# Performance work log

Hardware: AMD Instinct MI355X
Metric: run time of the kernel (lower is better)

The kernel has to match this reference:

```python
import jax, jax.numpy as jnp
import numpy as np

B, S, H, NH = 4, 2048, 2048, 16
HD = H // NH  # 128


def setup_inputs() -> dict:
    key = jax.random.key(0)
    ks = jax.random.split(key, 9)
    s = lambda fan_in: 1.0 / np.sqrt(fan_in)
    return {
        "hidden_state": jax.random.normal(ks[0], (B, S, H), dtype=jnp.float32),
        # Linear weights stored as [in, out]
        "w_q": jax.random.uniform(ks[1], (H, H), jnp.float32, -s(H), s(H)),
        "b_q": jax.random.uniform(ks[2], (H,), jnp.float32, -s(H), s(H)),
        "w_k": jax.random.uniform(ks[3], (H, HD), jnp.float32, -s(H), s(H)),
        "b_k": jax.random.uniform(ks[4], (HD,), jnp.float32, -s(H), s(H)),
        "w_v": jax.random.uniform(ks[5], (H, HD), jnp.float32, -s(H), s(H)),
        "b_v": jax.random.uniform(ks[6], (HD,), jnp.float32, -s(H), s(H)),
        "w_o": jax.random.uniform(ks[7], (H, H), jnp.float32, -s(H), s(H)),
        "b_o": jax.random.uniform(ks[8], (H,), jnp.float32, -s(H), s(H)),
    }


def reference(hidden_state, w_q, b_q, w_k, b_k, w_v, b_v, w_o, b_o):
    b = hidden_state.shape[0]
    q = hidden_state @ w_q + b_q                       # [B,S,H]
    k = hidden_state @ w_k + b_k                       # [B,S,HD] (single KV head)
    v = hidden_state @ w_v + b_v                       # [B,S,HD]
    q = q.reshape(b, -1, NH, HD).transpose(0, 2, 1, 3)  # [B,NH,S,HD]
    scale = jnp.sqrt(jnp.float32(HD))
    scores = jnp.einsum("bhqd,bkd->bhqk", q, k) / scale  # [B,NH,S,S]
    probs = jax.nn.softmax(scores, axis=-1)
    out = jnp.einsum("bhqk,bkd->bhqd", probs, v)        # [B,NH,S,HD]
    # Faithful to original: transpose(-1,-2) (NOT transpose(1,2)) then view
    out = jnp.swapaxes(out, -1, -2).reshape(b, -1, HD * NH)  # [B,S,H]
    return out @ w_o + b_o
```

## Files before the change

### kernel.cpp

```cpp
#include <hip/hip_runtime.h>
#include <math.h>


#define BATCH 4
#define SLEN 2048
#define HDIM 2048
#define NHEADS 16
#define HD 128

typedef __bf16 bf16x8 __attribute__((ext_vector_type(8)));
typedef float f32x4 __attribute__((ext_vector_type(4)));

__device__ __forceinline__ void gload_lds16(const void* g, void* l) {
    __builtin_amdgcn_global_load_lds(
        (const __attribute__((address_space(1))) void*)g,
        (__attribute__((address_space(3))) void*)l, 16, 0, 0);
}

__device__ __forceinline__ int xcd_swizzle(int bid, int nwg) {
    int cpx = nwg >> 3;
    return (bid & 7) * cpx + (bid >> 3);
}

__global__ void conv_bf16(const float* __restrict__ in, __bf16* __restrict__ out) {
    int i = (blockIdx.x * 256 + threadIdx.x) * 8;
    float4 a = *reinterpret_cast<const float4*>(in + i);
    float4 b = *reinterpret_cast<const float4*>(in + i + 4);
    bf16x8 o;
    o[0] = (__bf16)a.x; o[1] = (__bf16)a.y; o[2] = (__bf16)a.z; o[3] = (__bf16)a.w;
    o[4] = (__bf16)b.x; o[5] = (__bf16)b.y; o[6] = (__bf16)b.z; o[7] = (__bf16)b.w;
    *reinterpret_cast<bf16x8*>(out + i) = o;
}

__global__ void transpose_conv(const float* __restrict__ in, __bf16* __restrict__ out,
                               int R, int C) {
    __shared__ float tile[32][33];
    int c0 = blockIdx.x * 32, r0 = blockIdx.y * 32;
    int tr = threadIdx.x >> 5, tc = threadIdx.x & 31;
#pragma unroll
    for (int i = 0; i < 4; ++i)
        tile[tr + i * 8][tc] = in[(size_t)(r0 + tr + i * 8) * C + c0 + tc];
    __syncthreads();
#pragma unroll
    for (int i = 0; i < 4; ++i)
        out[(size_t)(c0 + tr + i * 8) * R + r0 + tc] = (__bf16)tile[tc][tr + i * 8];
}

template <int MODE>
__global__ __launch_bounds__(256) void gemm_bt(
    const __bf16* __restrict__ A, const __bf16* __restrict__ BT,
    const float* __restrict__ bias, const float* __restrict__ bias2,
    void* __restrict__ Cout, void* __restrict__ Cout2,
    int M, int N, int K, int nbx)
{
    __shared__ __bf16 As[128 * 64];
    __shared__ __bf16 Bs[128 * 64];
    const int t = threadIdx.x;
    const int lane = t & 63;
    const int w = t >> 6;
    const int wr = w >> 1, wc = w & 1;
    const int id = xcd_swizzle(blockIdx.x, gridDim.x);
    const int m0 = (id / nbx) << 7, n0 = (id % nbx) << 7;

    f32x4 acc[4][4] = {};
    const int l8 = (lane & 7) * 8;
    const int lr = lane >> 3;

    for (int k0 = 0; k0 < K; k0 += 64) {
        __syncthreads();
#pragma unroll
        for (int i = 0; i < 4; ++i) {
            int c = w * 4 + i;
            int row = c * 8 + lr;
            gload_lds16(A + (size_t)(m0 + row) * K + k0 + l8, (char*)As + c * 1024);
            gload_lds16(BT + (size_t)(n0 + row) * K + k0 + l8, (char*)Bs + c * 1024);
        }
        __syncthreads();
#pragma unroll
        for (int ks = 0; ks < 2; ++ks) {
            bf16x8 a[4], b[4];
#pragma unroll
            for (int i = 0; i < 4; ++i) {
                a[i] = *reinterpret_cast<const bf16x8*>(
                    As + (wr * 64 + i * 16 + (lane & 15)) * 64 + ks * 32 + (lane >> 4) * 8);
                b[i] = *reinterpret_cast<const bf16x8*>(
                    Bs + (wc * 64 + i * 16 + (lane & 15)) * 64 + ks * 32 + (lane >> 4) * 8);
            }
#pragma unroll
            for (int i = 0; i < 4; ++i)
#pragma unroll
                for (int j = 0; j < 4; ++j)
                    acc[i][j] = __builtin_amdgcn_mfma_f32_16x16x32_bf16(
                        a[i], b[j], acc[i][j], 0, 0, 0);
        }
    }

    const int col_l = lane & 15, rgrp = lane >> 4;
#pragma unroll
    for (int j = 0; j < 4; ++j) {
        int col = n0 + wc * 64 + j * 16 + col_l;
        float bv;
        if (MODE == 3)
            bv = (col < HD) ? bias[col] : bias2[col - HD];
        else
            bv = bias[col];
#pragma unroll
        for (int i = 0; i < 4; ++i) {
            int rowb = m0 + wr * 64 + i * 16 + rgrp * 4;
#pragma unroll
            for (int r = 0; r < 4; ++r) {
                float v = acc[i][j][r] + bv;
                int row = rowb + r;
                if (MODE == 0)
                    ((float*)Cout)[(size_t)row * N + col] = v;
                else if (MODE == 1)
                    ((__bf16*)Cout)[(size_t)row * N + col] = (__bf16)v;
                else {
                    if (col < HD)
                        ((__bf16*)Cout)[(size_t)row * HD + col] = (__bf16)v;
                    else
                        ((__bf16*)Cout2)[((size_t)(row >> 11) * HD + (col - HD)) * SLEN
                                         + (row & (SLEN - 1))] = (__bf16)v;
                }
            }
        }
    }
}

__attribute__((amdgpu_waves_per_eu(2, 4)))
__global__ __launch_bounds__(512) void mqa_attn_mfma(
    const __bf16* __restrict__ Q,
    const __bf16* __restrict__ K,
    const __bf16* __restrict__ VT,
    __bf16* __restrict__ T)
{
    __shared__ __align__(16) __bf16 smem[40960];
    __bf16* KsB = smem;
    __bf16* VtB = smem + 16384;
    __bf16* PsB = smem + 32768;

    const int t = threadIdx.x;
    const int lane = t & 63;
    const int w = t >> 6;
    const int bid = xcd_swizzle(blockIdx.x, gridDim.x);
    const int qb = bid & 15;
    const int nh = (bid >> 4) & 15;
    const int b = bid >> 8;
    const int q0 = qb << 7;

    const int cl = lane & 15;
    const int rg = lane >> 4;

    const float scale = 0.08838834764831845f;

    bf16x8 qf[4];
    {
        const __bf16* qrow = Q + (size_t)(b * SLEN + q0 + w * 16 + cl) * HDIM
                             + nh * HD + rg * 8;
#pragma unroll
        for (int ks = 0; ks < 4; ++ks) {
            bf16x8 raw = *reinterpret_cast<const bf16x8*>(qrow + ks * 32);
#pragma unroll
            for (int j = 0; j < 8; ++j)
                qf[ks][j] = (__bf16)((float)raw[j] * scale);
        }
    }

    f32x4 O[8] = {};
    float m[4], l[4];
#pragma unroll
    for (int r = 0; r < 4; ++r) { m[r] = -__builtin_inff(); l[r] = 0.f; }

    const int k_row0 = (w * 2) * 4 + (lane >> 4);
    const int k_cc0  = lane & 15;
    const int v_row0 = (w * 2) * 8 + (lane >> 3);
    const int v_cc0  = lane & 7;

#define STAGE_KV(TILE, BUF)                                                     \
    do {                                                                        \
        int kk_ = (TILE) * 64;                                                  \
        _Pragma("unroll")                                                       \
        for (int j = 0; j < 2; ++j) {                                           \
            int idx = w * 2 + j;                                                \
            int row = k_row0 + j * 4;                                           \
            int cc  = k_cc0 ^ (row & 7);                                        \
            gload_lds16(K + (size_t)(b * SLEN + kk_ + row) * HD + cc * 8,       \
                        (char*)(KsB + (BUF) * 8192) + idx * 1024);              \
        }                                                                       \
        _Pragma("unroll")                                                       \
        for (int j = 0; j < 2; ++j) {                                           \
            int idx = w * 2 + j;                                                \
            int row = v_row0 + j * 8;                                           \
            int cc  = v_cc0 ^ (row & 7);                                        \
            gload_lds16(VT + (size_t)(b * HD + row) * SLEN + kk_ + cc * 8,      \
                        (char*)(VtB + (BUF) * 8192) + idx * 1024);              \
        }                                                                       \
    } while (0)

    STAGE_KV(0, 0);
    __syncthreads();

    int buf = 0;
    const int NT = SLEN / 64;
    for (int tt = 0; tt < NT; ++tt) {
        if (tt + 1 < NT) STAGE_KV(tt + 1, buf ^ 1);

        const __bf16* Kb_ = KsB + buf * 8192;
        const __bf16* Vb_ = VtB + buf * 8192;

        f32x4 s[4] = {};
        __builtin_amdgcn_s_setprio(1);
#pragma unroll
        for (int cb = 0; cb < 4; ++cb) {
            const int row = cb * 16 + cl;
            const __bf16* kr = Kb_ + row * 128;
            const int sw = row & 7;
#pragma unroll
            for (int ks = 0; ks < 4; ++ks) {
                bf16x8 kf = *reinterpret_cast<const bf16x8*>(
                    kr + (((ks * 4 + rg) ^ sw) << 3));
                s[cb] = __builtin_amdgcn_mfma_f32_16x16x32_bf16(qf[ks], kf, s[cb], 0, 0, 0);
            }
        }
        __builtin_amdgcn_s_setprio(0);

        float tmax[4], mx = 0.f;
#pragma unroll
        for (int r = 0; r < 4; ++r) {
            float tm = fmaxf(fmaxf(s[0][r], s[1][r]), fmaxf(s[2][r], s[3][r]));
            tm = fmaxf(tm, __shfl_xor(tm, 1));
            tm = fmaxf(tm, __shfl_xor(tm, 2));
            tm = fmaxf(tm, __shfl_xor(tm, 4));
            tm = fmaxf(tm, __shfl_xor(tm, 8));
            tmax[r] = tm;
            mx = fmaxf(mx, tm - m[r]);
        }
        if (__any(mx > 8.f)) {
#pragma unroll
            for (int r = 0; r < 4; ++r) {
                float mn = fmaxf(m[r], tmax[r]);
                float alpha = __expf(m[r] - mn);
                m[r] = mn;
                l[r] *= alpha;
#pragma unroll
                for (int dcb = 0; dcb < 8; ++dcb) O[dcb][r] *= alpha;
            }
        }
        float rs[4] = {0.f, 0.f, 0.f, 0.f};
#pragma unroll
        for (int cb = 0; cb < 4; ++cb)
#pragma unroll
            for (int r = 0; r < 4; ++r) {
                float p = __expf(s[cb][r] - m[r]);
                rs[r] += p;
                int row = rg * 4 + r;
                int col = (cb * 16 + cl) ^ ((row & 7) << 3);
                PsB[w * 1024 + row * 64 + col] = (__bf16)p;
            }
#pragma unroll
        for (int r = 0; r < 4; ++r) {
            float v = rs[r];
            v += __shfl_xor(v, 1);
            v += __shfl_xor(v, 2);
            v += __shfl_xor(v, 4);
            v += __shfl_xor(v, 8);
            l[r] += v;
        }

        bf16x8 pf[2];
#pragma unroll
        for (int ks = 0; ks < 2; ++ks)
            pf[ks] = *reinterpret_cast<const bf16x8*>(
                PsB + w * 1024 + cl * 64 + (((ks * 4 + rg) ^ (cl & 7)) << 3));
        __builtin_amdgcn_s_setprio(1);
#pragma unroll
        for (int dcb = 0; dcb < 8; ++dcb) {
            const int row = dcb * 16 + cl;
            const __bf16* vr = Vb_ + row * 64;
            const int sw = row & 7;
#pragma unroll
            for (int ks = 0; ks < 2; ++ks) {
                bf16x8 vf = *reinterpret_cast<const bf16x8*>(
                    vr + (((ks * 4 + rg) ^ sw) << 3));
                O[dcb] = __builtin_amdgcn_mfma_f32_16x16x32_bf16(pf[ks], vf, O[dcb], 0, 0, 0);
            }
        }
        __builtin_amdgcn_s_setprio(0);

        __syncthreads();
        buf ^= 1;
    }
#undef STAGE_KV

    __bf16 (*Eb)[136] = reinterpret_cast<__bf16(*)[136]>(smem);
    float invl[4];
#pragma unroll
    for (int r = 0; r < 4; ++r) invl[r] = 1.0f / l[r];
#pragma unroll
    for (int dcb = 0; dcb < 8; ++dcb)
#pragma unroll
        for (int r = 0; r < 4; ++r)
            Eb[dcb * 16 + cl][w * 16 + rg * 4 + r] = (__bf16)(O[dcb][r] * invl[r]);
    __syncthreads();
#pragma unroll
    for (int i = 0; i < 4; ++i) {
        int id = i * 512 + t;
        int d = id >> 4, c = id & 15;
        float4 v = *reinterpret_cast<const float4*>(&Eb[d][c * 8]);
        *reinterpret_cast<float4*>(
            T + (size_t)(b * HDIM + nh * HD + d) * SLEN + q0 + c * 8) = v;
    }
}

extern "C" void kernel_launch(void* const* d_in, const int* in_sizes, int n_in,
                              void* d_out, int out_size, void* d_ws, size_t ws_size,
                              hipStream_t stream) {
    const float* hs  = (const float*)d_in[0];
    const float* w_q = (const float*)d_in[1];
    const float* b_q = (const float*)d_in[2];
    const float* w_k = (const float*)d_in[3];
    const float* b_k = (const float*)d_in[4];
    const float* w_v = (const float*)d_in[5];
    const float* b_v = (const float*)d_in[6];
    const float* w_o = (const float*)d_in[7];
    const float* b_o = (const float*)d_in[8];

    const int M = BATCH * SLEN;
    const size_t MH = (size_t)M * HDIM;

    __bf16* hs_b = (__bf16*)d_out;
    __bf16* Qb   = hs_b + MH;

    char* p = (char*)d_ws;
    __bf16* wqT = (__bf16*)p;             p += (size_t)HDIM * HDIM * 2;
    __bf16* woT = (__bf16*)p;             p += (size_t)HDIM * HDIM * 2;
    __bf16* wkT = (__bf16*)p;             p += (size_t)HD * HDIM * 2;
    __bf16* wvT = (__bf16*)p;             p += (size_t)HD * HDIM * 2;
    __bf16* Kb  = (__bf16*)p;             p += (size_t)M * HD * 2;
    __bf16* VTb = (__bf16*)p;             p += (size_t)M * HD * 2;
    __bf16* Tb  = (__bf16*)p;

    dim3 blk(256);

    conv_bf16<<<dim3(MH / (256 * 8)), blk, 0, stream>>>(hs, hs_b);
    transpose_conv<<<dim3(HDIM / 32, HDIM / 32), blk, 0, stream>>>(w_q, wqT, HDIM, HDIM);
    transpose_conv<<<dim3(HD / 32, HDIM / 32), blk, 0, stream>>>(w_k, wkT, HDIM, HD);
    transpose_conv<<<dim3(HD / 32, HDIM / 32), blk, 0, stream>>>(w_v, wvT, HDIM, HD);
    transpose_conv<<<dim3(HDIM / 32, HDIM / 32), blk, 0, stream>>>(w_o, woT, HDIM, HDIM);

    gemm_bt<1><<<dim3(16 * (M / 128)), blk, 0, stream>>>(
        hs_b, wqT, b_q, nullptr, Qb, nullptr, M, HDIM, HDIM, 16);
    gemm_bt<3><<<dim3(2 * (M / 128)), blk, 0, stream>>>(
        hs_b, wkT, b_k, b_v, Kb, VTb, M, 2 * HD, HDIM, 2);

    mqa_attn_mfma<<<dim3(BATCH * NHEADS * (SLEN / 128)), dim3(512), 0, stream>>>(
        Qb, Kb, VTb, Tb);

    gemm_bt<0><<<dim3(16 * (M / 128)), blk, 0, stream>>>(
        Tb, woT, b_o, nullptr, d_out, nullptr, M, HDIM, HDIM, 16);
}
```

Baseline: 644.0 us.

## Fuse Q/K/V projections into one GEMM and defer softmax row-sum reduction

The Q projection and the K/V projection GEMMs are merged into a single launch over a concatenated 2304-wide weight (wkT and wvT are now placed right after wqT), with a three-way epilogue that routes each column range to Q, K, or transposed V. This removes a launch and the poorly occupied 256-column K/V GEMM. In the attention kernel, the cross-lane shuffle for the row max now runs only when a rescale is triggered, and the row-sum shuffle is moved out of the loop to run once at the end. The lazy-rescale check now uses per-lane maxima rather than full-row maxima, so rescale decisions can differ slightly between lanes of a row.

```diff
diff --git a/kernel.cpp b/kernel.cpp
--- a/kernel.cpp
+++ b/kernel.cpp
@@ -50,7 +50,8 @@
 __global__ __launch_bounds__(256) void gemm_bt(
     const __bf16* __restrict__ A, const __bf16* __restrict__ BT,
     const float* __restrict__ bias, const float* __restrict__ bias2,
-    void* __restrict__ Cout, void* __restrict__ Cout2,
+    const float* __restrict__ bias3,
+    void* __restrict__ Cout, void* __restrict__ Cout2, void* __restrict__ Cout3,
     int M, int N, int K, int nbx)
 {
     __shared__ __bf16 As[128 * 64];
@@ -100,8 +101,10 @@
     for (int j = 0; j < 4; ++j) {
         int col = n0 + wc * 64 + j * 16 + col_l;
         float bv;
-        if (MODE == 3)
-            bv = (col < HD) ? bias[col] : bias2[col - HD];
+        if (MODE == 4)
+            bv = (col < HDIM) ? bias[col]
+               : (col < HDIM + HD) ? bias2[col - HDIM]
+               : bias3[col - HDIM - HD];
         else
             bv = bias[col];
 #pragma unroll
@@ -113,13 +116,13 @@
                 int row = rowb + r;
                 if (MODE == 0)
                     ((float*)Cout)[(size_t)row * N + col] = v;
-                else if (MODE == 1)
-                    ((__bf16*)Cout)[(size_t)row * N + col] = (__bf16)v;
                 else {
-                    if (col < HD)
-                        ((__bf16*)Cout)[(size_t)row * HD + col] = (__bf16)v;
+                    if (col < HDIM)
+                        ((__bf16*)Cout)[(size_t)row * HDIM + col] = (__bf16)v;
+                    else if (col < HDIM + HD)
+                        ((__bf16*)Cout2)[(size_t)row * HD + (col - HDIM)] = (__bf16)v;
                     else
-                        ((__bf16*)Cout2)[((size_t)(row >> 11) * HD + (col - HD)) * SLEN
+                        ((__bf16*)Cout3)[((size_t)(row >> 11) * HD + (col - HDIM - HD)) * SLEN
                                          + (row & (SLEN - 1))] = (__bf16)v;
                 }
             }
@@ -167,9 +170,9 @@
     }
 
     f32x4 O[8] = {};
-    float m[4], l[4];
-#pragma unroll
-    for (int r = 0; r < 4; ++r) { m[r] = -__builtin_inff(); l[r] = 0.f; }
+    float m[4], lacc[4];
+#pragma unroll
+    for (int r = 0; r < 4; ++r) { m[r] = -__builtin_inff(); lacc[r] = 0.f; }
 
     const int k_row0 = (w * 2) * 4 + (lane >> 4);
     const int k_cc0  = lane & 15;
@@ -224,48 +227,40 @@
         }
         __builtin_amdgcn_s_setprio(0);
 
-        float tmax[4], mx = 0.f;
+        float lmax[4];
+        float mx = -1e30f;
 #pragma unroll
         for (int r = 0; r < 4; ++r) {
             float tm = fmaxf(fmaxf(s[0][r], s[1][r]), fmaxf(s[2][r], s[3][r]));
-            tm = fmaxf(tm, __shfl_xor(tm, 1));
-            tm = fmaxf(tm, __shfl_xor(tm, 2));
-            tm = fmaxf(tm, __shfl_xor(tm, 4));
-            tm = fmaxf(tm, __shfl_xor(tm, 8));
-            tmax[r] = tm;
+            lmax[r] = tm;
             mx = fmaxf(mx, tm - m[r]);
         }
         if (__any(mx > 8.f)) {
 #pragma unroll
             for (int r = 0; r < 4; ++r) {
-                float mn = fmaxf(m[r], tmax[r]);
+                float tm = lmax[r];
+                tm = fmaxf(tm, __shfl_xor(tm, 1));
+                tm = fmaxf(tm, __shfl_xor(tm, 2));
+                tm = fmaxf(tm, __shfl_xor(tm, 4));
+                tm = fmaxf(tm, __shfl_xor(tm, 8));
+                float mn = fmaxf(m[r], tm);
                 float alpha = __expf(m[r] - mn);
                 m[r] = mn;
-                l[r] *= alpha;
+                lacc[r] *= alpha;
 #pragma unroll
                 for (int dcb = 0; dcb < 8; ++dcb) O[dcb][r] *= alpha;
             }
         }
-        float rs[4] = {0.f, 0.f, 0.f, 0.f};
 #pragma unroll
         for (int cb = 0; cb < 4; ++cb)
 #pragma unroll
             for (int r = 0; r < 4; ++r) {
                 float p = __expf(s[cb][r] - m[r]);
-                rs[r] += p;
+                lacc[r] += p;
                 int row = rg * 4 + r;
                 int col = (cb * 16 + cl) ^ ((row & 7) << 3);
                 PsB[w * 1024 + row * 64 + col] = (__bf16)p;
             }
-#pragma unroll
-        for (int r = 0; r < 4; ++r) {
-            float v = rs[r];
-            v += __shfl_xor(v, 1);
-            v += __shfl_xor(v, 2);
-            v += __shfl_xor(v, 4);
-            v += __shfl_xor(v, 8);
-            l[r] += v;
-        }
 
         bf16x8 pf[2];
 #pragma unroll
@@ -292,10 +287,17 @@
     }
 #undef STAGE_KV
 
+    float invl[4];
+#pragma unroll
+    for (int r = 0; r < 4; ++r) {
+        float v = lacc[r];
+        v += __shfl_xor(v, 1);
+        v += __shfl_xor(v, 2);
+        v += __shfl_xor(v, 4);
+        v += __shfl_xor(v, 8);
+        invl[r] = 1.0f / v;
+    }
     __bf16 (*Eb)[136] = reinterpret_cast<__bf16(*)[136]>(smem);
-    float invl[4];
-#pragma unroll
-    for (int r = 0; r < 4; ++r) invl[r] = 1.0f / l[r];
 #pragma unroll
     for (int dcb = 0; dcb < 8; ++dcb)
 #pragma unroll
@@ -333,9 +335,9 @@
 
     char* p = (char*)d_ws;
     __bf16* wqT = (__bf16*)p;             p += (size_t)HDIM * HDIM * 2;
-    __bf16* woT = (__bf16*)p;             p += (size_t)HDIM * HDIM * 2;
     __bf16* wkT = (__bf16*)p;             p += (size_t)HD * HDIM * 2;
     __bf16* wvT = (__bf16*)p;             p += (size_t)HD * HDIM * 2;
+    __bf16* woT = (__bf16*)p;             p += (size_t)HDIM * HDIM * 2;
     __bf16* Kb  = (__bf16*)p;             p += (size_t)M * HD * 2;
     __bf16* VTb = (__bf16*)p;             p += (size_t)M * HD * 2;
     __bf16* Tb  = (__bf16*)p;
@@ -348,14 +350,12 @@
     transpose_conv<<<dim3(HD / 32, HDIM / 32), blk, 0, stream>>>(w_v, wvT, HDIM, HD);
     transpose_conv<<<dim3(HDIM / 32, HDIM / 32), blk, 0, stream>>>(w_o, woT, HDIM, HDIM);
 
-    gemm_bt<1><<<dim3(16 * (M / 128)), blk, 0, stream>>>(
-        hs_b, wqT, b_q, nullptr, Qb, nullptr, M, HDIM, HDIM, 16);
-    gemm_bt<3><<<dim3(2 * (M / 128)), blk, 0, stream>>>(
-        hs_b, wkT, b_k, b_v, Kb, VTb, M, 2 * HD, HDIM, 2);
+    gemm_bt<4><<<dim3(18 * (M / 128)), blk, 0, stream>>>(
+        hs_b, wqT, b_q, b_k, b_v, Qb, Kb, VTb, M, 2304, HDIM, 18);
 
     mqa_attn_mfma<<<dim3(BATCH * NHEADS * (SLEN / 128)), dim3(512), 0, stream>>>(
         Qb, Kb, VTb, Tb);
 
     gemm_bt<0><<<dim3(16 * (M / 128)), blk, 0, stream>>>(
-        Tb, woT, b_o, nullptr, d_out, nullptr, M, HDIM, HDIM, 16);
-}
+        Tb, woT, b_o, nullptr, nullptr, d_out, nullptr, nullptr, M, HDIM, HDIM, 16);
+}
```

Measured after the change: 567.0 us. 1.14x faster.
